# Performance work log

Measured on AMD Instinct MI355X. Metric: run time of the kernel, lower is better.

Reference implementation:

```python
import jax, jax.numpy as jnp
import numpy as np

K = 20
EPS = 1e-5

def _lrelu(x):
    return jnp.where(x >= 0, x, 0.2 * x)

def _bn(x, g, b, m, v, axis=1):
    shp = [1] * x.ndim
    shp[axis] = -1
    scale = (g / jnp.sqrt(v + EPS)).reshape(shp)
    return (x - m.reshape(shp)) * scale + b.reshape(shp)

def _graph_feature(x, k):
    # x: [B, C, N] -> [B, 2C, N, k]  (kNN in feature space, concat(x_j - x_i, x_i))
    xx = jnp.sum(x * x, axis=1)                        # [B, N]
    inner = jnp.einsum('bcn,bcm->bnm', x, x)           # [B, N, N]
    neg_dist = 2.0 * inner - xx[:, :, None] - xx[:, None, :]
    _, idx = jax.lax.top_k(neg_dist, k)                # [B, N, k] nearest neighbors
    xt = jnp.transpose(x, (0, 2, 1))                   # [B, N, C]
    nb = jax.vmap(lambda f, i: f[i])(xt, idx)          # [B, N, k, C]
    center = jnp.broadcast_to(xt[:, :, None, :], nb.shape)
    feat = jnp.concatenate([nb - center, center], axis=-1)  # [B, N, k, 2C]
    return jnp.transpose(feat, (0, 3, 1, 2))

def _edge_block(x, w, g, b, m, v):
    # EdgeConv: graph feature -> 1x1 conv -> BN -> LeakyReLU -> max over k
    f = _graph_feature(x, K)                           # [B, 2C, N, k]
    y = jnp.einsum('oc,bcnk->bonk', w, f)
    y = _lrelu(_bn(y, g, b, m, v, 1))
    return jnp.max(y, axis=-1)                         # [B, O, N]


def setup_inputs() -> dict:
    key = jax.random.key(0)
    ks = iter(jax.random.split(key, 64))
    def randn(*s, scale=1.0):
        return jax.random.normal(next(ks), s, dtype=jnp.float32) * scale
    def unif(*s):
        return jax.random.uniform(next(ks), s, dtype=jnp.float32, minval=0.5, maxval=1.5)
    d = {}
    d['x'] = randn(16, 3, 1024)
    # conv / linear weights (fan-in scaled)
    for name, o, c in [('w1', 64, 6), ('w2', 64, 128), ('w3', 128, 128),
                       ('w4', 256, 256), ('w5', 1024, 512),
                       ('wl1', 512, 2048), ('wl2', 256, 512), ('wl3', 101, 256)]:
        d[name] = randn(o, c, scale=1.0 / np.sqrt(c))
    d['bl2'] = randn(256, scale=0.02)
    d['bl3'] = randn(101, scale=0.02)
    # BN params (eval-mode running stats)
    for i, c in [('1', 64), ('2', 64), ('3', 128), ('4', 256), ('5', 1024), ('6', 512), ('7', 256)]:
        d['g' + i] = 1.0 + randn(c, scale=0.1)
        d['b' + i] = randn(c, scale=0.1)
        d['m' + i] = randn(c, scale=0.1)
        d['v' + i] = unif(c)
    return d


def reference(x, w1, g1, b1, m1, v1, w2, g2, b2, m2, v2, w3, g3, b3, m3, v3,
              w4, g4, b4, m4, v4, w5, g5, b5, m5, v5,
              wl1, g6, b6, m6, v6, wl2, bl2, g7, b7, m7, v7, wl3, bl3):
    x1 = _edge_block(x,  w1, g1, b1, m1, v1)   # [B, 64, N]
    x2 = _edge_block(x1, w2, g2, b2, m2, v2)   # [B, 64, N]
    x3 = _edge_block(x2, w3, g3, b3, m3, v3)   # [B, 128, N]
    x4 = _edge_block(x3, w4, g4, b4, m4, v4)   # [B, 256, N]
    xc = jnp.concatenate([x1, x2, x3, x4], axis=1)           # [B, 512, N]
    y = _lrelu(_bn(jnp.einsum('oc,bcn->bon', w5, xc), g5, b5, m5, v5, 1))  # [B, 1024, N]
    p = jnp.concatenate([jnp.max(y, axis=-1), jnp.mean(y, axis=-1)], axis=1)  # [B, 2048]
    h = _lrelu(_bn(p @ wl1.T, g6, b6, m6, v6, 1))            # [B, 512]
    h = _lrelu(_bn(h @ wl2.T + bl2, g7, b7, m7, v7, 1))      # [B, 256]
    return h @ wl3.T + bl3                                   # [B, 101]
```

## Files before the change

### kernel.cpp

```cpp
#include <hip/hip_runtime.h>
#include <cstdint>
#include <cmath>

#define DI __device__ __forceinline__

constexpr int BB = 16;
constexpr int NN = 1024;
constexpr int KK = 20;
constexpr int NPT = BB*NN;
constexpr float EPSF = 1e-5f;
constexpr float NEGINF = -3.0e38f;

DI float lrelu(float x){ return x >= 0.f ? x : 0.2f * x; }
DI float dot4(const float4 a, const float4 b){ return a.x*b.x + a.y*b.y + a.z*b.z + a.w*b.w; }
DI unsigned short f2bf(float x){
    uint32_t u = __float_as_uint(x);
    uint32_t r = (u + 0x7fffu + ((u >> 16) & 1u)) >> 16;
    return (unsigned short)r;
}

typedef __attribute__((ext_vector_type(8))) short short8v;
typedef __attribute__((ext_vector_type(4))) float f32x4;

__global__ void k_transpose(const float* __restrict__ x, float* __restrict__ xt)
{
    int i = blockIdx.x * 256 + threadIdx.x;
    if (i >= NPT) return;
    int b = i >> 10, n = i & 1023;
    #pragma unroll
    for (int c = 0; c < 3; ++c) xt[i*3 + c] = x[(b*3 + c)*NN + n];
}

__global__ void k_sqnorm(const float* __restrict__ src, int stride, int C, float* __restrict__ xx)
{
    int i = blockIdx.x * 256 + threadIdx.x;
    if (i >= NPT) return;
    const float* r = src + (size_t)i * stride;
    float s = 0.f;
    for (int c = 0; c < C; ++c){ float v = r[c]; s += v * v; }
    xx[i] = s;
}

template<int C>
__global__ __launch_bounds__(1024, 4) void k_knn(const float* __restrict__ src, int stride,
                                                 const float* __restrict__ xx,
                                                 int* __restrict__ idxo)
{
    constexpr bool SMALL = (C == 3);
    constexpr int CG = SMALL ? 1 : (C / 4);
    constexpr int TS = SMALL ? 5 : C;
    __shared__ float tile[128 * TS];

    const int tid  = threadIdx.x;
    const int lane = tid & 63;
    const int wv   = __builtin_amdgcn_readfirstlane(tid >> 6);
    const int b  = blockIdx.x >> 4;
    const int q0 = (blockIdx.x & 15) << 6;
    const int qbase = b*NN + q0 + (wv << 2);

    const float* qp0 = src + (size_t)(qbase + 0)*stride;
    const float* qp1 = src + (size_t)(qbase + 1)*stride;
    const float* qp2 = src + (size_t)(qbase + 2)*stride;
    const float* qp3 = src + (size_t)(qbase + 3)*stride;

    float xxq[4];
    #pragma unroll
    for (int q = 0; q < 4; ++q) xxq[q] = xx[qbase + q];

    float val[4][16];

    #pragma unroll
    for (int t = 0; t < 8; ++t){
        __syncthreads();
        if constexpr (SMALL){
            for (int i = tid; i < 128*3; i += 1024){
                int row = i / 3, c = i % 3;
                tile[row*TS + c] = src[(size_t)(b*NN + t*128 + row)*stride + c];
            }
        } else {
            for (int i = tid; i < 128*CG; i += 1024){
                int row = i / CG, cg = i % CG;
                int p = cg ^ (row & (CG - 1));
                float4 v = *(const float4*)(src + (size_t)(b*NN + t*128 + row)*stride + cg*4);
                *(float4*)(tile + row*TS + p*4) = v;
            }
        }
        __syncthreads();

        float acc[4][2];
        #pragma unroll
        for (int q = 0; q < 4; ++q){ acc[q][0] = 0.f; acc[q][1] = 0.f; }

        if constexpr (SMALL){
            float c0a = tile[lane*TS+0], c0b = tile[lane*TS+1], c0c = tile[lane*TS+2];
            float c1a = tile[(64+lane)*TS+0], c1b = tile[(64+lane)*TS+1], c1c = tile[(64+lane)*TS+2];
            float q00 = qp0[0], q01 = qp0[1], q02 = qp0[2];
            float q10 = qp1[0], q11 = qp1[1], q12 = qp1[2];
            float q20 = qp2[0], q21 = qp2[1], q22 = qp2[2];
            float q30 = qp3[0], q31 = qp3[1], q32 = qp3[2];
            acc[0][0] = q00*c0a + q01*c0b + q02*c0c;  acc[0][1] = q00*c1a + q01*c1b + q02*c1c;
            acc[1][0] = q10*c0a + q11*c0b + q12*c0c;  acc[1][1] = q10*c1a + q11*c1b + q12*c1c;
            acc[2][0] = q20*c0a + q21*c0b + q22*c0c;  acc[2][1] = q20*c1a + q21*c1b + q22*c1c;
            acc[3][0] = q30*c0a + q31*c0b + q32*c0c;  acc[3][1] = q30*c1a + q31*c1b + q32*c1c;
        } else {
            const int sw = lane & (CG - 1);
            #pragma unroll 2
            for (int cg0 = 0; cg0 < CG; ++cg0){
                float4 cf0 = *(const float4*)(tile + lane*TS      + ((cg0 ^ sw) << 2));
                float4 cf1 = *(const float4*)(tile + (64+lane)*TS + ((cg0 ^ sw) << 2));
                float4 qf0 = *(const float4*)(qp0 + (cg0 << 2));
                float4 qf1 = *(const float4*)(qp1 + (cg0 << 2));
                float4 qf2 = *(const float4*)(qp2 + (cg0 << 2));
                float4 qf3 = *(const float4*)(qp3 + (cg0 << 2));
                acc[0][0] += dot4(qf0, cf0); acc[0][1] += dot4(qf0, cf1);
                acc[1][0] += dot4(qf1, cf0); acc[1][1] += dot4(qf1, cf1);
                acc[2][0] += dot4(qf2, cf0); acc[2][1] += dot4(qf2, cf1);
                acc[3][0] += dot4(qf3, cf0); acc[3][1] += dot4(qf3, cf1);
            }
        }
        float xxm0 = xx[b*NN + t*128 + lane];
        float xxm1 = xx[b*NN + t*128 + 64 + lane];
        #pragma unroll
        for (int q = 0; q < 4; ++q){
            val[q][2*t]   = 2.f*acc[q][0] - xxq[q] - xxm0;
            val[q][2*t+1] = 2.f*acc[q][1] - xxq[q] - xxm1;
        }
    }

    #pragma unroll
    for (int qq = 0; qq < 4; qq += 2){
        float s0[16], s1[16];
        #pragma unroll
        for (int j = 0; j < 16; ++j){ s0[j] = val[qq][j]; s1[j] = val[qq+1][j]; }

        #pragma unroll
        for (int k = 2; k <= 16; k <<= 1){
            #pragma unroll
            for (int jj = k >> 1; jj > 0; jj >>= 1){
                #pragma unroll
                for (int i = 0; i < 16; ++i){
                    int l = i ^ jj;
                    if (l > i){
                        bool up = ((i & k) == 0);
                        float a0 = s0[i], c0 = s0[l];
                        float mx0 = fmaxf(a0, c0), mn0 = fminf(a0, c0);
                        s0[i] = up ? mx0 : mn0;  s0[l] = up ? mn0 : mx0;
                        float a1 = s1[i], c1 = s1[l];
                        float mx1 = fmaxf(a1, c1), mn1 = fminf(a1, c1);
                        s1[i] = up ? mx1 : mn1;  s1[l] = up ? mn1 : mx1;
                    }
                }
            }
        }

        float T0 = NEGINF, T1 = NEGINF;
        for (int it = 0; it < 21; ++it){
            float m0 = s0[0], m1 = s1[0];
            #pragma unroll
            for (int d = 1; d < 64; d <<= 1){
                float p0 = __shfl_xor(m0, d);
                float p1 = __shfl_xor(m1, d);
                m0 = fmaxf(m0, p0);
                m1 = fmaxf(m1, p1);
            }
            T0 = m0; T1 = m1;
            unsigned long long mk0 = __ballot(s0[0] == m0);
            unsigned long long mk1 = __ballot(s1[0] == m1);
            bool a0 = (lane == __ffsll(mk0) - 1);
            bool a1 = (lane == __ffsll(mk1) - 1);
            #pragma unroll
            for (int j = 0; j < 15; ++j){
                s0[j] = a0 ? s0[j+1] : s0[j];
                s1[j] = a1 ? s1[j+1] : s1[j];
            }
            s0[15] = a0 ? NEGINF : s0[15];
            s1[15] = a1 ? NEGINF : s1[15];
        }

        #pragma unroll
        for (int h = 0; h < 2; ++h){
            const int q = qq + h;
            const float T = h ? T1 : T0;
            const int orow = (qbase + q) * KK;
            int cnt = 0;
            #pragma unroll
            for (int j = 0; j < 16; ++j) cnt += (val[q][j] > T) ? 1 : 0;
            int off = cnt;
            #pragma unroll
            for (int d = 1; d < 64; d <<= 1){
                int tt = __shfl_up(off, d);
                if (lane >= d) off += tt;
            }
            int total = __shfl(off, 63);
            int pos = orow + off - cnt;
            #pragma unroll
            for (int j = 0; j < 16; ++j){
                if (val[q][j] > T){ idxo[pos] = j*64 + lane; ++pos; }
            }
            if (total < KK){
                int rem = KK - total;
                int prior = 0;
                #pragma unroll
                for (int j = 0; j < 16; ++j){
                    unsigned long long mk = __ballot(val[q][j] == T);
                    int below = __popcll(mk & ((1ull << lane) - 1ull));
                    if ((val[q][j] == T) && (prior + below < rem))
                        idxo[orow + total + prior + below] = j*64 + lane;
                    prior += __popcll(mk);
                }
            }
        }
    }
}

__global__ void k_wprep(const float* __restrict__ w, int O, int C, float* __restrict__ wp)
{
    int i = blockIdx.x*256 + threadIdx.x;
    if (i >= O*C) return;
    int o = i / C, c = i % C;
    float a = w[o*2*C + c];
    float bq = w[o*2*C + C + c];
    wp[o*C + c]       = a;
    wp[(O + o)*C + c] = bq - a;
}

template<int K, int M2, int O, bool UB16>
__global__ __launch_bounds__(256) void k_uvgemm(const float* __restrict__ srcp,
    const float* __restrict__ wp,
    const float* __restrict__ g, const float* __restrict__ bp,
    const float* __restrict__ mp, const float* __restrict__ vp,
    float* __restrict__ ub, float* __restrict__ xcv)
{
    constexpr int LD = 136;
    __shared__ float wl[16*LD];
    __shared__ float xl[16*LD];
    const int tid = threadIdx.x;
    const int nt = blockIdx.x & 127;
    const int mt = blockIdx.x >> 7;
    const int to = tid >> 4, tn = tid & 15;

    float acc[8][8];
    #pragma unroll
    for (int i = 0; i < 8; ++i)
        #pragma unroll
        for (int j = 0; j < 8; ++j) acc[i][j] = 0.f;

    for (int c0 = 0; c0 < K; c0 += 16){
        __syncthreads();
        #pragma unroll
        for (int p = 0; p < 2; ++p){
            int fi = tid + (p << 8);
            int row = fi >> 2, cq = (fi & 3) << 2;
            float4 wv = *(const float4*)(wp + (size_t)(mt*128 + row)*K + c0 + cq);
            wl[(cq+0)*LD + row] = wv.x;
            wl[(cq+1)*LD + row] = wv.y;
            wl[(cq+2)*LD + row] = wv.z;
            wl[(cq+3)*LD + row] = wv.w;
            float4 xv = *(const float4*)(srcp + (size_t)(nt*128 + row)*512 + c0 + cq);
            xl[(cq+0)*LD + row] = xv.x;
            xl[(cq+1)*LD + row] = xv.y;
            xl[(cq+2)*LD + row] = xv.z;
            xl[(cq+3)*LD + row] = xv.w;
        }
        __syncthreads();
        #pragma unroll
        for (int cc = 0; cc < 16; ++cc){
            float4 a0 = *(const float4*)(wl + cc*LD + to*8);
            float4 a1 = *(const float4*)(wl + cc*LD + to*8 + 4);
            float4 b0 = *(const float4*)(xl + cc*LD + tn*8);
            float4 b1 = *(const float4*)(xl + cc*LD + tn*8 + 4);
            float av[8] = {a0.x,a0.y,a0.z,a0.w,a1.x,a1.y,a1.z,a1.w};
            float bv[8] = {b0.x,b0.y,b0.z,b0.w,b1.x,b1.y,b1.z,b1.w};
            #pragma unroll
            for (int i = 0; i < 8; ++i)
                #pragma unroll
                for (int j = 0; j < 8; ++j) acc[i][j] += av[i]*bv[j];
        }
    }

    const int mbase = mt*128 + to*8;
    const bool isu = mbase < O;
    float mult[8], add[8];
    #pragma unroll
    for (int i = 0; i < 8; ++i){
        int m = mbase + i;
        if (isu){
            float s = g[m] / sqrtf(vp[m] + EPSF);
            mult[i] = (s >= 0.f) ? 1.f : -1.f;
            add[i]  = 0.f;
        } else {
            int o = m - O;
            float s = g[o] / sqrtf(vp[o] + EPSF);
            mult[i] = s;
            add[i]  = bp[o] - mp[o]*s;
        }
    }
    #pragma unroll
    for (int j = 0; j < 8; ++j){
        int pt = nt*128 + tn*8 + j;
        float4 v0, v1;
        v0.x = fmaf(mult[0], acc[0][j], add[0]);
        v0.y = fmaf(mult[1], acc[1][j], add[1]);
        v0.z = fmaf(mult[2], acc[2][j], add[2]);
        v0.w = fmaf(mult[3], acc[3][j], add[3]);
        v1.x = fmaf(mult[4], acc[4][j], add[4]);
        v1.y = fmaf(mult[5], acc[5][j], add[5]);
        v1.z = fmaf(mult[6], acc[6][j], add[6]);
        v1.w = fmaf(mult[7], acc[7][j], add[7]);
        if (isu){
            if constexpr (UB16){
                union { unsigned short u[8]; uint4 v; } o;
                o.u[0] = f2bf(v0.x); o.u[1] = f2bf(v0.y); o.u[2] = f2bf(v0.z); o.u[3] = f2bf(v0.w);
                o.u[4] = f2bf(v1.x); o.u[5] = f2bf(v1.y); o.u[6] = f2bf(v1.z); o.u[7] = f2bf(v1.w);
                *(uint4*)((unsigned short*)ub + (size_t)pt*O + mbase) = o.v;
            } else {
                float* d = ub + (size_t)pt*O + mbase;
                *(float4*)(d)     = v0;
                *(float4*)(d + 4) = v1;
            }
        } else {
            float* d = xcv + (size_t)pt*512 + (mbase - O);
            *(float4*)(d)     = v0;
            *(float4*)(d + 4) = v1;
        }
    }
}

__global__ __launch_bounds__(256) void k_uv3(const float* __restrict__ xt,
    const float* __restrict__ wp,
    const float* __restrict__ g, const float* __restrict__ bp,
    const float* __restrict__ mp, const float* __restrict__ vp,
    float* __restrict__ ub, float* __restrict__ xcv)
{
    __shared__ float wpl[128*3];
    __shared__ float mult[128], add[128];
    const int tid = threadIdx.x;
    if (tid < 128){
        int m = tid;
        if (m < 64){
            float s = g[m] / sqrtf(vp[m] + EPSF);
            mult[m] = (s >= 0.f) ? 1.f : -1.f;
            add[m]  = 0.f;
        } else {
            int o = m - 64;
            float s = g[o] / sqrtf(vp[o] + EPSF);
            mult[m] = s;
            add[m]  = bp[o] - mp[o]*s;
        }
    }
    for (int i = tid; i < 128*3; i += 256) wpl[i] = wp[i];
    __syncthreads();

    const int ptl = tid >> 5, mg = tid & 31;
    const int m0 = mg * 4;
    const int pt = blockIdx.x*8 + ptl;
    float x0 = xt[pt*3+0], x1 = xt[pt*3+1], x2 = xt[pt*3+2];
    float4 v4;
    float tmp[4];
    #pragma unroll
    for (int r = 0; r < 4; ++r){
        int m = m0 + r;
        float a = wpl[m*3+0]*x0 + wpl[m*3+1]*x1 + wpl[m*3+2]*x2;
        tmp[r] = fmaf(mult[m], a, add[m]);
    }
    v4.x = tmp[0]; v4.y = tmp[1]; v4.z = tmp[2]; v4.w = tmp[3];
    if (m0 < 64) *(float4*)(ub + (size_t)pt*64 + m0) = v4;
    else         *(float4*)(xcv + (size_t)pt*512 + (m0 - 64)) = v4;
}

template<int O, bool UB16>
__global__ __launch_bounds__(256) void k_edgemax(const float* __restrict__ ub,
    const int* __restrict__ idxg,
    const float* __restrict__ g, const float* __restrict__ vp,
    float* __restrict__ xcv)
{
    constexpr int TPP = O / 4;
    constexpr int PPB = 256 / TPP;
    const int tid = threadIdx.x;
    const int pt  = blockIdx.x*PPB + tid / TPP;
    const int oq  = (tid % TPP) * 4;
    const int bb  = pt & ~(NN-1);

    int nb[KK];
    #pragma unroll
    for (int k = 0; k < KK; ++k) nb[k] = idxg[pt*KK + k];

    float4 mx;
    if constexpr (UB16){
        const unsigned short* ubh = (const unsigned short*)ub;
        uint2 r0 = *(const uint2*)(ubh + (size_t)(bb + nb[0])*O + oq);
        mx.x = __uint_as_float(r0.x << 16);
        mx.y = __uint_as_float(r0.x & 0xffff0000u);
        mx.z = __uint_as_float(r0.y << 16);
        mx.w = __uint_as_float(r0.y & 0xffff0000u);
        #pragma unroll
        for (int k = 1; k < KK; ++k){
            uint2 r = *(const uint2*)(ubh + (size_t)(bb + nb[k])*O + oq);
            mx.x = fmaxf(mx.x, __uint_as_float(r.x << 16));
            mx.y = fmaxf(mx.y, __uint_as_float(r.x & 0xffff0000u));
            mx.z = fmaxf(mx.z, __uint_as_float(r.y << 16));
            mx.w = fmaxf(mx.w, __uint_as_float(r.y & 0xffff0000u));
        }
    } else {
        mx = *(const float4*)(ub + (size_t)(bb + nb[0])*O + oq);
        #pragma unroll
        for (int k = 1; k < KK; ++k){
            float4 u = *(const float4*)(ub + (size_t)(bb + nb[k])*O + oq);
            mx.x = fmaxf(mx.x, u.x); mx.y = fmaxf(mx.y, u.y);
            mx.z = fmaxf(mx.z, u.z); mx.w = fmaxf(mx.w, u.w);
        }
    }
    float4 gv = *(const float4*)(g + oq);
    float4 vv = *(const float4*)(vp + oq);
    float4 as;
    as.x = fabsf(gv.x / sqrtf(vv.x + EPSF));
    as.y = fabsf(gv.y / sqrtf(vv.y + EPSF));
    as.z = fabsf(gv.z / sqrtf(vv.z + EPSF));
    as.w = fabsf(gv.w / sqrtf(vv.w + EPSF));
    float* d = xcv + (size_t)pt*512 + oq;
    float4 vr = *(const float4*)(d);
    float4 y;
    y.x = lrelu(fmaf(as.x, mx.x, vr.x));
    y.y = lrelu(fmaf(as.y, mx.y, vr.y));
    y.z = lrelu(fmaf(as.z, mx.z, vr.z));
    y.w = lrelu(fmaf(as.w, mx.w, vr.w));
    *(float4*)(d) = y;
}

__global__ void k_castbf(const float* __restrict__ s, unsigned short* __restrict__ d, int n8)
{
    int i = blockIdx.x*256 + threadIdx.x;
    if (i >= n8) return;
    const float4* sp = (const float4*)s + (size_t)i*2;
    float4 a = sp[0], b = sp[1];
    union { unsigned short u[8]; uint4 v; } o;
    o.u[0] = f2bf(a.x); o.u[1] = f2bf(a.y); o.u[2] = f2bf(a.z); o.u[3] = f2bf(a.w);
    o.u[4] = f2bf(b.x); o.u[5] = f2bf(b.y); o.u[6] = f2bf(b.z); o.u[7] = f2bf(b.w);
    *((uint4*)d + i) = o.v;
}

__global__ __launch_bounds__(256) void k_conv5mfma(const unsigned short* __restrict__ xcb,
    const unsigned short* __restrict__ w5b,
    const float* __restrict__ g, const float* __restrict__ bp,
    const float* __restrict__ mp, const float* __restrict__ vp,
    float* __restrict__ pmax, float* __restrict__ psum)
{
    __shared__ __align__(16) short lA[128*32];
    __shared__ __align__(16) short lB[128*32];
    __shared__ float scl[128], adl[128];
    __shared__ float red[2][128][2];

    const int tid = threadIdx.x;
    const int lane = tid & 63, wave = tid >> 6;
    const int wm = wave >> 1, wn = wave & 1;
    const int b  = blockIdx.x >> 6;
    const int mt = (blockIdx.x >> 3) & 7;
    const int nt = blockIdx.x & 7;

    if (tid < 128){
        int o = mt*128 + tid;
        float s = g[o] / sqrtf(vp[o] + EPSF);
        scl[tid] = s;
        adl[tid] = bp[o] - mp[o]*s;
    }

    f32x4 acc[4][4];
    #pragma unroll
    for (int i = 0; i < 4; ++i)
        #pragma unroll
        for (int j = 0; j < 4; ++j) acc[i][j] = (f32x4){0.f,0.f,0.f,0.f};

    const unsigned short* gA = w5b + (size_t)(mt*128)*512;
    const unsigned short* gB = xcb + (size_t)(b*1024 + nt*128)*512;

    for (int ks = 0; ks < 16; ++ks){
        __syncthreads();
        #pragma unroll
        for (int p = 0; p < 2; ++p){
            int off = p*256 + tid;
            int row = off >> 2;
            int slot = off & 3;
            int ssl = slot ^ (row & 3);
            *(uint4*)(lA + row*32 + ssl*8) = *(const uint4*)(gA + (size_t)row*512 + ks*32 + slot*8);
            *(uint4*)(lB + row*32 + ssl*8) = *(const uint4*)(gB + (size_t)row*512 + ks*32 + slot*8);
        }
        __syncthreads();

        short8v afr[4], bfr[4];
        #pragma unroll
        for (int i = 0; i < 4; ++i){
            int row = wm*64 + i*16 + (lane & 15);
            int sl  = (lane >> 4) ^ (row & 3);
            afr[i] = *(const short8v*)(lA + row*32 + sl*8);
        }
        #pragma unroll
        for (int j = 0; j < 4; ++j){
            int row = wn*64 + j*16 + (lane & 15);
            int sl  = (lane >> 4) ^ (row & 3);
            bfr[j] = *(const short8v*)(lB + row*32 + sl*8);
        }
        #pragma unroll
        for (int i = 0; i < 4; ++i)
            #pragma unroll
            for (int j = 0; j < 4; ++j)
                acc[i][j] = __builtin_amdgcn_mfma_f32_16x16x32_bf16(afr[i], bfr[j], acc[i][j], 0, 0, 0);
    }

    float emx[4][4], esm[4][4];
    #pragma unroll
    for (int i = 0; i < 4; ++i){
        #pragma unroll
        for (int r = 0; r < 4; ++r){
            int m_loc = wm*64 + i*16 + (lane >> 4)*4 + r;
            float s = scl[m_loc], t = adl[m_loc];
            float mx = NEGINF, sm = 0.f;
            #pragma unroll
            for (int j = 0; j < 4; ++j){
                float y = lrelu(fmaf(acc[i][j][r], s, t));
                mx = fmaxf(mx, y); sm += y;
            }
            #pragma unroll
            for (int d = 1; d < 16; d <<= 1){
                mx = fmaxf(mx, __shfl_xor(mx, d));
                sm += __shfl_xor(sm, d);
            }
            emx[i][r] = mx; esm[i][r] = sm;
        }
    }
    if ((lane & 15) == 0){
        #pragma unroll
        for (int i = 0; i < 4; ++i)
            #pragma unroll
            for (int r = 0; r < 4; ++r){
                int m_loc = wm*64 + i*16 + (lane >> 4)*4 + r;
                red[wn][m_loc][0] = emx[i][r];
                red[wn][m_loc][1] = esm[i][r];
            }
    }
    __syncthreads();
    if (tid < 128){
        float mx = fmaxf(red[0][tid][0], red[1][tid][0]);
        float sm = red[0][tid][1] + red[1][tid][1];
        int o = mt*128 + tid;
        pmax[(size_t)(b*NN + o)*8 + nt] = mx;
        psum[(size_t)(b*NN + o)*8 + nt] = sm;
    }
}

__global__ void k_poolfin(const float* __restrict__ pmax, const float* __restrict__ psum,
                          float* __restrict__ p)
{
    int i = blockIdx.x*256 + threadIdx.x;
    if (i >= NPT) return;
    int b = i >> 10, o = i & 1023;
    float mx = NEGINF, sm = 0.f;
    #pragma unroll
    for (int t = 0; t < 8; ++t){ mx = fmaxf(mx, pmax[(size_t)i*8 + t]); sm += psum[(size_t)i*8 + t]; }
    p[b*2048 + o]        = mx;
    p[b*2048 + 1024 + o] = sm * (1.f/1024.f);
}

template<int IN, int O, bool HASBN, bool HASBIAS>
__global__ void k_fc(const float* __restrict__ in, const float* __restrict__ W,
                     const float* __restrict__ bias,
                     const float* __restrict__ g, const float* __restrict__ bp,
                     const float* __restrict__ mp, const float* __restrict__ vp,
                     float* __restrict__ out)
{
    int i = blockIdx.x*256 + threadIdx.x;
    if (i >= BB*O) return;
    int b = i / O, o = i % O;
    const float* wr = W  + (size_t)o*IN;
    const float* ir = in + (size_t)b*IN;
    float s = 0.f;
    #pragma unroll 4
    for (int c = 0; c < IN; c += 4){
        float4 a = *(const float4*)(wr + c);
        float4 x = *(const float4*)(ir + c);
        s += dot4(a, x);
    }
    if (HASBIAS) s += bias[o];
    if (HASBN){
        float sc = g[o] / sqrtf(vp[o] + EPSF);
        s = (s - mp[o])*sc + bp[o];
        s = lrelu(s);
    }
    out[(size_t)b*O + o] = s;
}

extern "C" void kernel_launch(void* const* d_in, const int* in_sizes, int n_in,
                              void* d_out, int out_size, void* d_ws, size_t ws_size,
                              hipStream_t stream)
{
    (void)in_sizes; (void)n_in; (void)out_size; (void)ws_size;
    const float* x   = (const float*)d_in[0];
    const float* w1  = (const float*)d_in[1];
    const float* w2  = (const float*)d_in[2];
    const float* w3  = (const float*)d_in[3];
    const float* w4  = (const float*)d_in[4];
    const float* w5  = (const float*)d_in[5];
    const float* wl1 = (const float*)d_in[6];
    const float* wl2 = (const float*)d_in[7];
    const float* wl3 = (const float*)d_in[8];
    const float* bl2 = (const float*)d_in[9];
    const float* bl3 = (const float*)d_in[10];
    const float* g1 = (const float*)d_in[11]; const float* b1 = (const float*)d_in[12];
    const float* m1 = (const float*)d_in[13]; const float* v1 = (const float*)d_in[14];
    const float* g2 = (const float*)d_in[15]; const float* b2 = (const float*)d_in[16];
    const float* m2 = (const float*)d_in[17]; const float* v2 = (const float*)d_in[18];
    const float* g3 = (const float*)d_in[19]; const float* b3 = (const float*)d_in[20];
    const float* m3 = (const float*)d_in[21]; const float* v3 = (const float*)d_in[22];
    const float* g4 = (const float*)d_in[23]; const float* b4 = (const float*)d_in[24];
    const float* m4 = (const float*)d_in[25]; const float* v4 = (const float*)d_in[26];
    const float* g5 = (const float*)d_in[27]; const float* b5 = (const float*)d_in[28];
    const float* m5 = (const float*)d_in[29]; const float* v5 = (const float*)d_in[30];
    const float* g6 = (const float*)d_in[31]; const float* b6 = (const float*)d_in[32];
    const float* m6 = (const float*)d_in[33]; const float* v6 = (const float*)d_in[34];
    const float* g7 = (const float*)d_in[35]; const float* b7 = (const float*)d_in[36];
    const float* m7 = (const float*)d_in[37]; const float* v7 = (const float*)d_in[38];

    float* wsf  = (float*)d_ws;
    float* xt0  = wsf;
    float* xc   = xt0 + 49152;
    float* xx   = xc + 8388608;
    int*   idx  = (int*)(xx + 16384);
    float* pmax = (float*)(idx + 327680);
    float* psum = pmax + 131072;
    float* p    = psum + 131072;
    float* h1   = p + 32768;
    float* h2   = h1 + 8192;
    float* ub   = h2 + 4096;
    float* wp   = ub + 4194304;
    unsigned short* xcb = (unsigned short*)ub;
    unsigned short* w5b = (unsigned short*)idx;

    k_transpose<<<64, 256, 0, stream>>>(x, xt0);

    k_sqnorm<<<64, 256, 0, stream>>>(xt0, 3, 3, xx);
    k_knn<3><<<256, 1024, 0, stream>>>(xt0, 3, xx, idx);
    k_wprep<<<1, 256, 0, stream>>>(w1, 64, 3, wp);
    k_uv3<<<2048, 256, 0, stream>>>(xt0, wp, g1, b1, m1, v1, ub, xc);
    k_edgemax<64, false><<<1024, 256, 0, stream>>>(ub, idx, g1, v1, xc);

    k_sqnorm<<<64, 256, 0, stream>>>(xc, 512, 64, xx);
    k_knn<64><<<256, 1024, 0, stream>>>(xc, 512, xx, idx);
    k_wprep<<<16, 256, 0, stream>>>(w2, 64, 64, wp);
    k_uvgemm<64, 128, 64, false><<<128, 256, 0, stream>>>(xc, wp, g2, b2, m2, v2, ub, xc + 64);
    k_edgemax<64, false><<<1024, 256, 0, stream>>>(ub, idx, g2, v2, xc + 64);

    k_sqnorm<<<64, 256, 0, stream>>>(xc + 64, 512, 64, xx);
    k_knn<64><<<256, 1024, 0, stream>>>(xc + 64, 512, xx, idx);
    k_wprep<<<32, 256, 0, stream>>>(w3, 128, 64, wp);
    k_uvgemm<64, 256, 128, false><<<256, 256, 0, stream>>>(xc + 64, wp, g3, b3, m3, v3, ub, xc + 128);
    k_edgemax<128, false><<<2048, 256, 0, stream>>>(ub, idx, g3, v3, xc + 128);

    k_sqnorm<<<64, 256, 0, stream>>>(xc + 128, 512, 128, xx);
    k_knn<128><<<256, 1024, 0, stream>>>(xc + 128, 512, xx, idx);
    k_wprep<<<128, 256, 0, stream>>>(w4, 256, 128, wp);
    k_uvgemm<128, 512, 256, true><<<512, 256, 0, stream>>>(xc + 128, wp, g4, b4, m4, v4, ub, xc + 256);
    k_edgemax<256, true><<<4096, 256, 0, stream>>>(ub, idx, g4, v4, xc + 256);

    k_castbf<<<4096, 256, 0, stream>>>(xc, xcb, 1048576);
    k_castbf<<<256, 256, 0, stream>>>(w5, w5b, 65536);
    k_conv5mfma<<<1024, 256, 0, stream>>>(xcb, w5b, g5, b5, m5, v5, pmax, psum);
    k_poolfin<<<64, 256, 0, stream>>>(pmax, psum, p);

    k_fc<2048, 512, true,  false><<<32, 256, 0, stream>>>(p,  wl1, nullptr, g6, b6, m6, v6, h1);
    k_fc<512,  256, true,  true ><<<16, 256, 0, stream>>>(h1, wl2, bl2,     g7, b7, m7, v7, h2);
    k_fc<256,  101, false, true ><<<7,  256, 0, stream>>>(h2, wl3, bl3, nullptr, nullptr, nullptr, nullptr, (float*)d_out);
}
```

Measured before the change: 619.5 us.

## Double-buffer kNN candidate tiles and use DPP wave max in top-k selection

The kNN kernel for C>3 now stages candidate tiles in two LDS buffers. The next tile is prefetched into registers while the current one is processed, which removes one barrier per tile and overlaps global loads with compute. The 64-lane max reduction in the iterative top-k extraction uses DPP row operations for the intra-row steps instead of a full shuffle chain. Selection is now done one query at a time instead of two interleaved, which lowers register pressure but gives less instruction-level parallelism. The extra LDS buffer and prefetch registers may reduce occupancy.

```diff
diff --git a/kernel.cpp b/kernel.cpp
--- a/kernel.cpp
+++ b/kernel.cpp
@@ -19,6 +19,16 @@
     return (unsigned short)r;
 }
 
+DI float wave_max64(float v){
+    v = fmaxf(v, __int_as_float(__builtin_amdgcn_mov_dpp(__float_as_int(v), 0x121, 0xF, 0xF, true)));
+    v = fmaxf(v, __int_as_float(__builtin_amdgcn_mov_dpp(__float_as_int(v), 0x122, 0xF, 0xF, true)));
+    v = fmaxf(v, __int_as_float(__builtin_amdgcn_mov_dpp(__float_as_int(v), 0x124, 0xF, 0xF, true)));
+    v = fmaxf(v, __int_as_float(__builtin_amdgcn_mov_dpp(__float_as_int(v), 0x128, 0xF, 0xF, true)));
+    v = fmaxf(v, __shfl_xor(v, 16));
+    v = fmaxf(v, __shfl_xor(v, 32));
+    return v;
+}
+
 typedef __attribute__((ext_vector_type(8))) short short8v;
 typedef __attribute__((ext_vector_type(4))) float f32x4;
 
@@ -49,7 +59,9 @@
     constexpr bool SMALL = (C == 3);
     constexpr int CG = SMALL ? 1 : (C / 4);
     constexpr int TS = SMALL ? 5 : C;
-    __shared__ float tile[128 * TS];
+    constexpr int NBUF = SMALL ? 1 : 2;
+    constexpr int LPT = SMALL ? 1 : (128*CG/1024);
+    __shared__ float tile[NBUF][128 * TS];
 
     const int tid  = threadIdx.x;
     const int lane = tid & 63;
@@ -69,45 +81,68 @@
 
     float val[4][16];
 
-    #pragma unroll
-    for (int t = 0; t < 8; ++t){
-        __syncthreads();
-        if constexpr (SMALL){
+    if constexpr (SMALL){
+        #pragma unroll
+        for (int t = 0; t < 8; ++t){
+            __syncthreads();
             for (int i = tid; i < 128*3; i += 1024){
                 int row = i / 3, c = i % 3;
-                tile[row*TS + c] = src[(size_t)(b*NN + t*128 + row)*stride + c];
-            }
-        } else {
-            for (int i = tid; i < 128*CG; i += 1024){
-                int row = i / CG, cg = i % CG;
-                int p = cg ^ (row & (CG - 1));
-                float4 v = *(const float4*)(src + (size_t)(b*NN + t*128 + row)*stride + cg*4);
-                *(float4*)(tile + row*TS + p*4) = v;
-            }
-        }
-        __syncthreads();
-
-        float acc[4][2];
-        #pragma unroll
-        for (int q = 0; q < 4; ++q){ acc[q][0] = 0.f; acc[q][1] = 0.f; }
-
-        if constexpr (SMALL){
-            float c0a = tile[lane*TS+0], c0b = tile[lane*TS+1], c0c = tile[lane*TS+2];
-            float c1a = tile[(64+lane)*TS+0], c1b = tile[(64+lane)*TS+1], c1c = tile[(64+lane)*TS+2];
+                tile[0][row*TS + c] = src[(size_t)(b*NN + t*128 + row)*stride + c];
+            }
+            __syncthreads();
+            float c0a = tile[0][lane*TS+0], c0b = tile[0][lane*TS+1], c0c = tile[0][lane*TS+2];
+            float c1a = tile[0][(64+lane)*TS+0], c1b = tile[0][(64+lane)*TS+1], c1c = tile[0][(64+lane)*TS+2];
             float q00 = qp0[0], q01 = qp0[1], q02 = qp0[2];
             float q10 = qp1[0], q11 = qp1[1], q12 = qp1[2];
             float q20 = qp2[0], q21 = qp2[1], q22 = qp2[2];
             float q30 = qp3[0], q31 = qp3[1], q32 = qp3[2];
-            acc[0][0] = q00*c0a + q01*c0b + q02*c0c;  acc[0][1] = q00*c1a + q01*c1b + q02*c1c;
-            acc[1][0] = q10*c0a + q11*c0b + q12*c0c;  acc[1][1] = q10*c1a + q11*c1b + q12*c1c;
-            acc[2][0] = q20*c0a + q21*c0b + q22*c0c;  acc[2][1] = q20*c1a + q21*c1b + q22*c1c;
-            acc[3][0] = q30*c0a + q31*c0b + q32*c0c;  acc[3][1] = q30*c1a + q31*c1b + q32*c1c;
-        } else {
+            float xxm0 = xx[b*NN + t*128 + lane];
+            float xxm1 = xx[b*NN + t*128 + 64 + lane];
+            val[0][2*t]   = 2.f*(q00*c0a + q01*c0b + q02*c0c) - xxq[0] - xxm0;
+            val[0][2*t+1] = 2.f*(q00*c1a + q01*c1b + q02*c1c) - xxq[0] - xxm1;
+            val[1][2*t]   = 2.f*(q10*c0a + q11*c0b + q12*c0c) - xxq[1] - xxm0;
+            val[1][2*t+1] = 2.f*(q10*c1a + q11*c1b + q12*c1c) - xxq[1] - xxm1;
+            val[2][2*t]   = 2.f*(q20*c0a + q21*c0b + q22*c0c) - xxq[2] - xxm0;
+            val[2][2*t+1] = 2.f*(q20*c1a + q21*c1b + q22*c1c) - xxq[2] - xxm1;
+            val[3][2*t]   = 2.f*(q30*c0a + q31*c0b + q32*c0c) - xxq[3] - xxm0;
+            val[3][2*t+1] = 2.f*(q30*c1a + q31*c1b + q32*c1c) - xxq[3] - xxm1;
+        }
+    } else {
+        float4 nx[LPT];
+        #pragma unroll
+        for (int k = 0; k < LPT; ++k){
+            int i = tid + k*1024;
+            int row = i / CG, cg = i % CG;
+            nx[k] = *(const float4*)(src + (size_t)(b*NN + row)*stride + cg*4);
+        }
+        #pragma unroll
+        for (int k = 0; k < LPT; ++k){
+            int i = tid + k*1024;
+            int row = i / CG, cg = i % CG;
+            int p = cg ^ (row & (CG - 1));
+            *(float4*)(&tile[0][row*TS + p*4]) = nx[k];
+        }
+
+        for (int t = 0; t < 8; ++t){
+            __syncthreads();
+            if (t < 7){
+                #pragma unroll
+                for (int k = 0; k < LPT; ++k){
+                    int i = tid + k*1024;
+                    int row = i / CG, cg = i % CG;
+                    nx[k] = *(const float4*)(src + (size_t)(b*NN + (t+1)*128 + row)*stride + cg*4);
+                }
+            }
+            const float* tb = tile[t & 1];
+
+            float acc[4][2];
+            #pragma unroll
+            for (int q = 0; q < 4; ++q){ acc[q][0] = 0.f; acc[q][1] = 0.f; }
             const int sw = lane & (CG - 1);
             #pragma unroll 2
             for (int cg0 = 0; cg0 < CG; ++cg0){
-                float4 cf0 = *(const float4*)(tile + lane*TS      + ((cg0 ^ sw) << 2));
-                float4 cf1 = *(const float4*)(tile + (64+lane)*TS + ((cg0 ^ sw) << 2));
+                float4 cf0 = *(const float4*)(tb + lane*TS      + ((cg0 ^ sw) << 2));
+                float4 cf1 = *(const float4*)(tb + (64+lane)*TS + ((cg0 ^ sw) << 2));
                 float4 qf0 = *(const float4*)(qp0 + (cg0 << 2));
                 float4 qf1 = *(const float4*)(qp1 + (cg0 << 2));
                 float4 qf2 = *(const float4*)(qp2 + (cg0 << 2));
@@ -117,22 +152,34 @@
                 acc[2][0] += dot4(qf2, cf0); acc[2][1] += dot4(qf2, cf1);
                 acc[3][0] += dot4(qf3, cf0); acc[3][1] += dot4(qf3, cf1);
             }
-        }
-        float xxm0 = xx[b*NN + t*128 + lane];
-        float xxm1 = xx[b*NN + t*128 + 64 + lane];
-        #pragma unroll
-        for (int q = 0; q < 4; ++q){
-            val[q][2*t]   = 2.f*acc[q][0] - xxq[q] - xxm0;
-            val[q][2*t+1] = 2.f*acc[q][1] - xxq[q] - xxm1;
-        }
-    }
-
-    #pragma unroll
-    for (int qq = 0; qq < 4; qq += 2){
-        float s0[16], s1[16];
-        #pragma unroll
-        for (int j = 0; j < 16; ++j){ s0[j] = val[qq][j]; s1[j] = val[qq+1][j]; }
-
+            float xxm0 = xx[b*NN + t*128 + lane];
+            float xxm1 = xx[b*NN + t*128 + 64 + lane];
+            #pragma unroll
+            for (int q = 0; q < 4; ++q){
+                val[q][2*t]   = 2.f*acc[q][0] - xxq[q] - xxm0;
+                val[q][2*t+1] = 2.f*acc[q][1] - xxq[q] - xxm1;
+            }
+
+            if (t < 7){
+                float* wb = &tile[(t+1) & 1][0];
+                #pragma unroll
+                for (int k = 0; k < LPT; ++k){
+                    int i = tid + k*1024;
+                    int row = i / CG, cg = i % CG;
+                    int p = cg ^ (row & (CG - 1));
+                    *(float4*)(&wb[row*TS + p*4]) = nx[k];
+                }
+            }
+        }
+    }
+
+    #pragma unroll
+    for (int q = 0; q < 4; ++q){
+        const int orow = (qbase + q) * KK;
+
+        float s[16];
+        #pragma unroll
+        for (int j = 0; j < 16; ++j) s[j] = val[q][j];
         #pragma unroll
         for (int k = 2; k <= 16; k <<= 1){
             #pragma unroll
@@ -141,73 +188,53 @@
                 for (int i = 0; i < 16; ++i){
                     int l = i ^ jj;
                     if (l > i){
+                        float a = s[i], c = s[l];
+                        float mx = fmaxf(a, c), mn = fminf(a, c);
                         bool up = ((i & k) == 0);
-                        float a0 = s0[i], c0 = s0[l];
-                        float mx0 = fmaxf(a0, c0), mn0 = fminf(a0, c0);
-                        s0[i] = up ? mx0 : mn0;  s0[l] = up ? mn0 : mx0;
-                        float a1 = s1[i], c1 = s1[l];
-                        float mx1 = fmaxf(a1, c1), mn1 = fminf(a1, c1);
-                        s1[i] = up ? mx1 : mn1;  s1[l] = up ? mn1 : mx1;
+                        s[i] = up ? mx : mn;
+                        s[l] = up ? mn : mx;
                     }
                 }
             }
         }
 
-        float T0 = NEGINF, T1 = NEGINF;
+        float T = NEGINF;
         for (int it = 0; it < 21; ++it){
-            float m0 = s0[0], m1 = s1[0];
-            #pragma unroll
-            for (int d = 1; d < 64; d <<= 1){
-                float p0 = __shfl_xor(m0, d);
-                float p1 = __shfl_xor(m1, d);
-                m0 = fmaxf(m0, p0);
-                m1 = fmaxf(m1, p1);
-            }
-            T0 = m0; T1 = m1;
-            unsigned long long mk0 = __ballot(s0[0] == m0);
-            unsigned long long mk1 = __ballot(s1[0] == m1);
-            bool a0 = (lane == __ffsll(mk0) - 1);
-            bool a1 = (lane == __ffsll(mk1) - 1);
-            #pragma unroll
-            for (int j = 0; j < 15; ++j){
-                s0[j] = a0 ? s0[j+1] : s0[j];
-                s1[j] = a1 ? s1[j+1] : s1[j];
-            }
-            s0[15] = a0 ? NEGINF : s0[15];
-            s1[15] = a1 ? NEGINF : s1[15];
-        }
-
-        #pragma unroll
-        for (int h = 0; h < 2; ++h){
-            const int q = qq + h;
-            const float T = h ? T1 : T0;
-            const int orow = (qbase + q) * KK;
-            int cnt = 0;
-            #pragma unroll
-            for (int j = 0; j < 16; ++j) cnt += (val[q][j] > T) ? 1 : 0;
-            int off = cnt;
-            #pragma unroll
-            for (int d = 1; d < 64; d <<= 1){
-                int tt = __shfl_up(off, d);
-                if (lane >= d) off += tt;
-            }
-            int total = __shfl(off, 63);
-            int pos = orow + off - cnt;
+            float m = wave_max64(s[0]);
+            T = m;
+            unsigned long long mk = __ballot(s[0] == m);
+            int wl = __ffsll(mk) - 1;
+            bool adv = (lane == wl);
+            #pragma unroll
+            for (int j = 0; j < 15; ++j) s[j] = adv ? s[j+1] : s[j];
+            s[15] = adv ? NEGINF : s[15];
+        }
+
+        int cnt = 0;
+        #pragma unroll
+        for (int j = 0; j < 16; ++j) cnt += (val[q][j] > T) ? 1 : 0;
+        int off = cnt;
+        #pragma unroll
+        for (int d = 1; d < 64; d <<= 1){
+            int tt = __shfl_up(off, d);
+            if (lane >= d) off += tt;
+        }
+        int total = __shfl(off, 63);
+        int pos = orow + off - cnt;
+        #pragma unroll
+        for (int j = 0; j < 16; ++j){
+            if (val[q][j] > T){ idxo[pos] = j*64 + lane; ++pos; }
+        }
+        if (total < KK){
+            int rem = KK - total;
+            int prior = 0;
             #pragma unroll
             for (int j = 0; j < 16; ++j){
-                if (val[q][j] > T){ idxo[pos] = j*64 + lane; ++pos; }
-            }
-            if (total < KK){
-                int rem = KK - total;
-                int prior = 0;
-                #pragma unroll
-                for (int j = 0; j < 16; ++j){
-                    unsigned long long mk = __ballot(val[q][j] == T);
-                    int below = __popcll(mk & ((1ull << lane) - 1ull));
-                    if ((val[q][j] == T) && (prior + below < rem))
-                        idxo[orow + total + prior + below] = j*64 + lane;
-                    prior += __popcll(mk);
-                }
+                unsigned long long mk = __ballot(val[q][j] == T);
+                int below = __popcll(mk & ((1ull << lane) - 1ull));
+                if ((val[q][j] == T) && (prior + below < rem))
+                    idxo[orow + total + prior + below] = j*64 + lane;
+                prior += __popcll(mk);
             }
         }
     }
```

Result: faster. 581.7 us (-6.1%).
